# Kernel tuning notes

Measured on AMD Instinct MI355X. Metric: run time of the kernel, lower is better.

The kernel has to match this reference:

```python
import jax, jax.numpy as jnp
import numpy as np

TOP_K = 2  # num_experts_per_tok


def setup_inputs() -> dict:
    key = jax.random.key(0)
    ks = jax.random.split(key, 7)
    B, S, D = 4, 4096, 512
    E, H = 16, 4 * 512  # num_experts, expert hidden dim
    s_in = 1.0 / np.sqrt(D)
    s_h = 1.0 / np.sqrt(H)
    return {
        "x": jax.random.normal(ks[0], (B, S, D), dtype=jnp.float32),
        "Wg": jax.random.normal(ks[1], (D, E), dtype=jnp.float32) * s_in,
        "bg": jnp.zeros((E,), dtype=jnp.float32),
        "W1": jax.random.normal(ks[2], (E, D, H), dtype=jnp.float32) * s_in,
        "b1": jnp.zeros((E, H), dtype=jnp.float32),
        "W2": jax.random.normal(ks[3], (E, H, D), dtype=jnp.float32) * s_h,
        "b2": jnp.zeros((E, D), dtype=jnp.float32),
    }


def reference(x, Wg, bg, W1, b1, W2, b2):
    B, S, D = x.shape
    E = W1.shape[0]
    xf = x.reshape(-1, D)  # [T, D], T = B*S

    # 1. routing: top-k gate logits, softmax over the selected k (in fp32)
    logits = xf @ Wg + bg                      # [T, E]
    w, idx = jax.lax.top_k(logits, TOP_K)      # [T, K]
    w = jax.nn.softmax(w.astype(jnp.float32), axis=1).astype(x.dtype)

    # 2. combine weights per (token, expert): sum of gate weights where selected
    onehot = jax.nn.one_hot(idx, E, dtype=x.dtype)   # [T, K, E]
    combine = jnp.einsum("tk,tke->te", w, onehot)    # [T, E]

    # 3. per-expert FFN (Linear -> GELU(exact) -> Linear), masked combine.
    # Fixed loop over experts (structural, not data dim); tokens not routed to
    # expert e get combine weight 0, matching the sort/segment/scatter original.
    out = jnp.zeros_like(xf)
    for e in range(E):
        h = jax.nn.gelu(xf @ W1[e] + b1[e], approximate=False)  # [T, H]
        y = h @ W2[e] + b2[e]                                   # [T, D]
        out = out + combine[:, e:e + 1] * y

    return out.reshape(B, S, D)
```

## Files before the change

### kernel.cpp

```cpp
#include <hip/hip_runtime.h>
#include <hip/hip_bf16.h>

#define T_TOK 16384
#define DDIM  512
#define NEXP  16
#define HDIM  2048
#define NSLOT (T_TOK * 2)
#define NHB   128

#define GBM 128
#define GBN 256
#define GBN2 128
#define BK  32
#define MAXTILE 272
#define TSLICE  136

typedef __attribute__((ext_vector_type(8))) short short8;
typedef __attribute__((ext_vector_type(4))) short short4v;
typedef __attribute__((ext_vector_type(4))) float f32x4;

__device__ inline short f2bf(float f) {
    __hip_bfloat16 h = __float2bfloat16(f);
    return *reinterpret_cast<short*>(&h);
}
__device__ inline float bf2f(short s) {
    unsigned u = ((unsigned)(unsigned short)s) << 16;
    union { unsigned u; float f; } c; c.u = u; return c.f;
}
__device__ inline float erf_fast(float x) {
    float ax = fabsf(x);
    float t = 1.0f / fmaf(0.3275911f, ax, 1.0f);
    float p = fmaf(fmaf(fmaf(fmaf(1.061405429f, t, -1.453152027f), t,
                  1.421413741f), t, -0.284496736f), t, 0.254829592f) * t;
    float r = 1.0f - p * __expf(-ax * ax);
    return copysignf(r, x);
}
__device__ inline float geluf(float v) {
    return 0.5f * v * (1.0f + erf_fast(v * 0.70710678118654752440f));
}
__device__ inline void gload16(const void* g, void* l) {
    __builtin_amdgcn_global_load_lds(
        (const __attribute__((address_space(1))) void*)g,
        (__attribute__((address_space(3))) void*)l, 16, 0, 0);
}
__device__ inline void xcd_decode(int lin, int nx, int tc, int& y, int& xn) {
    if ((tc & 7) == 0) {
        int tpx = tc >> 3;
        int k = lin & 7, j = lin >> 3;
        y = k * tpx + j % tpx;
        xn = j / tpx;
    } else {
        xn = lin % nx;
        y = lin / nx;
    }
}

__global__ __launch_bounds__(256) void gate_kernel(
    const float* __restrict__ x, const float* __restrict__ wg,
    const float* __restrict__ bg, int* __restrict__ tok_e,
    float* __restrict__ tok_w)
{
    int wv = threadIdx.x >> 6, lane = threadIdx.x & 63;
    int t = blockIdx.x * 4 + wv;
    int g = lane >> 4, q = lane & 15;
    const float* xr = x + (size_t)t * DDIM + g * 128;
    const float* wr = wg + (size_t)g * 128 * NEXP + q;
    double a0 = 0, a1 = 0, a2 = 0, a3 = 0;
#pragma unroll
    for (int c = 0; c < 8; ++c) {
        float4 v0 = ((const float4*)xr)[c * 4 + 0];
        float4 v1 = ((const float4*)xr)[c * 4 + 1];
        float4 v2 = ((const float4*)xr)[c * 4 + 2];
        float4 v3 = ((const float4*)xr)[c * 4 + 3];
        const float* wp = wr + c * 16 * NEXP;
        a0 += (double)v0.x * (double)wp[0 * NEXP];
        a1 += (double)v0.y * (double)wp[1 * NEXP];
        a2 += (double)v0.z * (double)wp[2 * NEXP];
        a3 += (double)v0.w * (double)wp[3 * NEXP];
        a0 += (double)v1.x * (double)wp[4 * NEXP];
        a1 += (double)v1.y * (double)wp[5 * NEXP];
        a2 += (double)v1.z * (double)wp[6 * NEXP];
        a3 += (double)v1.w * (double)wp[7 * NEXP];
        a0 += (double)v2.x * (double)wp[8 * NEXP];
        a1 += (double)v2.y * (double)wp[9 * NEXP];
        a2 += (double)v2.z * (double)wp[10 * NEXP];
        a3 += (double)v2.w * (double)wp[11 * NEXP];
        a0 += (double)v3.x * (double)wp[12 * NEXP];
        a1 += (double)v3.y * (double)wp[13 * NEXP];
        a2 += (double)v3.z * (double)wp[14 * NEXP];
        a3 += (double)v3.w * (double)wp[15 * NEXP];
    }
    double a = ((a0 + a1) + (a2 + a3));
    a += __shfl_xor(a, 16, 64);
    a += __shfl_xor(a, 32, 64);
    a += (double)bg[q];
    double v0 = a; int i0 = q;
#pragma unroll
    for (int s = 1; s < 16; s <<= 1) {
        double ov = __shfl_xor(v0, s, 64);
        int oi = __shfl_xor(i0, s, 64);
        if (ov > v0 || (ov == v0 && oi < i0)) { v0 = ov; i0 = oi; }
    }
    double m2 = (q == i0) ? -1e300 : a;
    double v1 = m2; int i1 = q;
#pragma unroll
    for (int s = 1; s < 16; s <<= 1) {
        double ov = __shfl_xor(v1, s, 64);
        int oi = __shfl_xor(i1, s, 64);
        if (ov > v1 || (ov == v1 && oi < i1)) { v1 = ov; i1 = oi; }
    }
    if (lane == 0) {
        float ex = expf((float)(v1 - v0));
        float w0 = 1.0f / (1.0f + ex);
        tok_e[2 * t] = i0; tok_e[2 * t + 1] = i1;
        tok_w[2 * t] = w0; tok_w[2 * t + 1] = ex * w0;
    }
}

__global__ __launch_bounds__(256) void hist_kernel(
    const int* __restrict__ tok_e, int* __restrict__ bhist)
{
    __shared__ int h[NEXP];
    if (threadIdx.x < NEXP) h[threadIdx.x] = 0;
    __syncthreads();
    atomicAdd(&h[tok_e[blockIdx.x * 256 + threadIdx.x]], 1);
    __syncthreads();
    if (threadIdx.x < NEXP) bhist[blockIdx.x * NEXP + threadIdx.x] = h[threadIdx.x];
}

__global__ void scan_kernel(const int* __restrict__ bhist, int* __restrict__ offs,
                            int* __restrict__ bbase, int* __restrict__ tile_e,
                            int* __restrict__ tile_m0)
{
    int tid = threadIdx.x;
    __shared__ int tot[NEXP];
    if (tid < NEXP) {
        int s = 0;
        for (int b = 0; b < NHB; ++b) s += bhist[b * NEXP + tid];
        tot[tid] = s;
    }
    __syncthreads();
    if (tid == 0) {
        int run = 0;
        for (int e = 0; e < NEXP; ++e) { offs[e] = run; run += tot[e]; }
        offs[NEXP] = run;
        int nt = 0;
        for (int e = 0; e < NEXP; ++e)
            for (int m = offs[e]; m < offs[e + 1]; m += GBM) {
                tile_e[nt] = e; tile_m0[nt] = m; ++nt;
            }
        offs[17] = nt;
    }
    __syncthreads();
    if (tid < NEXP) {
        int run = offs[tid];
        for (int b = 0; b < NHB; ++b) {
            bbase[b * NEXP + tid] = run;
            run += bhist[b * NEXP + tid];
        }
    }
}

__global__ __launch_bounds__(256) void scatter_kernel(
    const int* __restrict__ tok_e, const float* __restrict__ tok_w,
    const int* __restrict__ bbase, int* __restrict__ list_tok,
    float* __restrict__ list_w, int* __restrict__ pos_tk)
{
    __shared__ int h[NEXP];
    if (threadIdx.x < NEXP) h[threadIdx.x] = 0;
    __syncthreads();
    int s = blockIdx.x * 256 + threadIdx.x;
    int e = tok_e[s];
    int r = atomicAdd(&h[e], 1);
    int pos = bbase[blockIdx.x * NEXP + e] + r;
    list_tok[pos] = s >> 1;
    list_w[pos] = tok_w[s];
    pos_tk[s] = pos;
}


__global__ void cvt_bf16_kernel(const float* __restrict__ src, short* __restrict__ dst, int n4)
{
    int i = blockIdx.x * blockDim.x + threadIdx.x;
    int stride = gridDim.x * blockDim.x;
    for (; i < n4; i += stride) {
        float4 v = ((const float4*)src)[i];
        short4v o;
        o[0] = f2bf(v.x); o[1] = f2bf(v.y); o[2] = f2bf(v.z); o[3] = f2bf(v.w);
        ((short4v*)dst)[i] = o;
    }
}

__global__ void wtrans_kernel(const float* __restrict__ src, short* __restrict__ dst, int R, int C)
{
    __shared__ float t[32][33];
    int c0 = blockIdx.x * 32, r0 = blockIdx.y * 32;
    const float* s = src + (size_t)blockIdx.z * R * C;
    short* d = dst + (size_t)blockIdx.z * R * C;
    int cc = threadIdx.x & 31, rr = threadIdx.x >> 5;
#pragma unroll
    for (int pp = 0; pp < 4; ++pp)
        t[rr + pp * 8][cc] = s[(size_t)(r0 + rr + pp * 8) * C + c0 + cc];
    __syncthreads();
#pragma unroll
    for (int pp = 0; pp < 4; ++pp) {
        int c = rr + pp * 8;
        d[(size_t)(c0 + c) * R + r0 + cc] = f2bf(t[cc][c]);
    }
}


__global__ __launch_bounds__(512) void gemm1_kernel(
    const short* __restrict__ xbf, const short* __restrict__ w1t,
    const float* __restrict__ b1, const int* __restrict__ offs,
    const int* __restrict__ tile_e, const int* __restrict__ tile_m0,
    const int* __restrict__ list_tok, short* __restrict__ hbuf,
    int h0, int hlen, int t0, int tc)
{
    int ty, xn;
    xcd_decode((int)blockIdx.x, hlen / GBN, tc, ty, xn);
    int tb = t0 + ty;
    if (tb >= offs[17]) return;
    int e = tile_e[tb], m0 = tile_m0[tb];
    int rows = offs[e + 1] - m0; if (rows > GBM) rows = GBM;
    int n0 = xn * GBN;
    int tid = threadIdx.x, l = tid & 63, w = tid >> 6;

    __shared__ __align__(16) short As[3][GBM * BK];
    __shared__ __align__(16) short Bs[3][GBN * BK];
    __shared__ int ts[GBM];
    if (tid < GBM) ts[tid] = list_tok[m0 + (tid < rows ? tid : rows - 1)];
    __syncthreads();

    int arow = w * 16 + (l >> 2);
    int aslot = (l & 3) ^ ((arow >> 1) & 3);
    const short* gA = xbf + (size_t)ts[arow] * DDIM + aslot * 8;
    int brow0 = (w * 2 + 0) * 16 + (l >> 2);
    int brow1 = (w * 2 + 1) * 16 + (l >> 2);
    int bs0 = (l & 3) ^ ((brow0 >> 1) & 3);
    int bs1 = (l & 3) ^ ((brow1 >> 1) & 3);
    const short* gB0 = w1t + ((size_t)e * HDIM + (size_t)(h0 + n0 + brow0)) * DDIM + bs0 * 8;
    const short* gB1 = w1t + ((size_t)e * HDIM + (size_t)(h0 + n0 + brow1)) * DDIM + bs1 * 8;

    int l15 = l & 15, kq = l >> 4;
    int aoff[4], boff[4];
#pragma unroll
    for (int mi = 0; mi < 4; ++mi) {
        int R = (w >> 2) * 64 + mi * 16 + l15;
        aoff[mi] = R * BK + ((kq ^ ((R >> 1) & 3)) * 8);
    }
#pragma unroll
    for (int ni = 0; ni < 4; ++ni) {
        int S = (w & 3) * 64 + ni * 16 + l15;
        boff[ni] = S * BK + ((kq ^ ((S >> 1) & 3)) * 8);
    }

    f32x4 vzero = {0.0f, 0.0f, 0.0f, 0.0f};
    f32x4 acc[4][4];
#pragma unroll
    for (int i = 0; i < 4; ++i)
#pragma unroll
        for (int j = 0; j < 4; ++j) acc[i][j] = vzero;

#define STAGE1(T, B) {                                            \
        gload16(gA  + (T) * BK, &As[B][w * 512]);                 \
        gload16(gB0 + (T) * BK, &Bs[B][(w * 2 + 0) * 512]);       \
        gload16(gB1 + (T) * BK, &Bs[B][(w * 2 + 1) * 512]); }

    const int nt = DDIM / BK;
    STAGE1(0, 0);
    STAGE1(1, 1);
    int cb = 0, sb = 2;
#pragma unroll 1
    for (int t = 0; t < nt; ++t) {
        if (t < nt - 1) asm volatile("s_waitcnt vmcnt(3)" ::: "memory");
        else            asm volatile("s_waitcnt vmcnt(0)" ::: "memory");
        __builtin_amdgcn_s_barrier();
        __builtin_amdgcn_sched_barrier(0);
        if (t + 2 < nt) STAGE1(t + 2, sb);
        const short* Ab = &As[cb][0];
        const short* Bb = &Bs[cb][0];
        short8 af[4], bv[4];
#pragma unroll
        for (int mi = 0; mi < 4; ++mi) af[mi] = *(const short8*)(Ab + aoff[mi]);
#pragma unroll
        for (int ni = 0; ni < 4; ++ni) bv[ni] = *(const short8*)(Bb + boff[ni]);
        __builtin_amdgcn_s_setprio(1);
#pragma unroll
        for (int mi = 0; mi < 4; ++mi)
#pragma unroll
            for (int ni = 0; ni < 4; ++ni)
                acc[mi][ni] = __builtin_amdgcn_mfma_f32_16x16x32_bf16(
                    af[mi], bv[ni], acc[mi][ni], 0, 0, 0);
        __builtin_amdgcn_s_setprio(0);
        cb = (cb == 2) ? 0 : cb + 1;
        sb = (sb == 2) ? 0 : sb + 1;
    }
#undef STAGE1

    int crow = (w >> 2) * 64 + (kq << 2);
    int ccol = (w & 3) * 64 + l15;
#pragma unroll
    for (int mi = 0; mi < 4; ++mi) {
#pragma unroll
        for (int ni = 0; ni < 4; ++ni) {
            int col = ccol + ni * 16;
            float bias = b1[e * HDIM + h0 + n0 + col];
#pragma unroll
            for (int j = 0; j < 4; ++j) {
                int row = crow + mi * 16 + j;
                if (row < rows) {
                    float v = acc[mi][ni][j] + bias;
                    hbuf[(size_t)(m0 + row) * hlen + (n0 + col)] = f2bf(geluf(v));
                }
            }
        }
    }
}

__global__ __launch_bounds__(512) void gemm2_kernel(
    const short* __restrict__ hbuf, const short* __restrict__ w2t,
    const float* __restrict__ b2, const int* __restrict__ offs,
    const int* __restrict__ tile_e, const int* __restrict__ tile_m0,
    const int* __restrict__ list_tok, const float* __restrict__ list_w,
    short* __restrict__ ybuf, float* __restrict__ out,
    int h0, int hlen, int mode, int t0, int tc)
{
    int ty, xn;
    xcd_decode((int)blockIdx.x, DDIM / GBN2, tc, ty, xn);
    int tb = t0 + ty;
    if (tb >= offs[17]) return;
    int e = tile_e[tb], m0 = tile_m0[tb];
    int rows = offs[e + 1] - m0; if (rows > GBM) rows = GBM;
    int n0 = xn * GBN2;
    int tid = threadIdx.x, l = tid & 63, w = tid >> 6;

    __shared__ __align__(16) short As[3][GBM * BK];
    __shared__ __align__(16) short Bs[3][GBN2 * BK];
    __shared__ int ts[GBM];
    __shared__ float lw[GBM];
    if (tid < GBM) {
        int idx = m0 + (tid < rows ? tid : rows - 1);
        ts[tid] = list_tok[idx];
        lw[tid] = list_w[idx];
    }
    __syncthreads();

    int arow = w * 16 + (l >> 2);
    int aslot = (l & 3) ^ ((arow >> 1) & 3);
    int aslotg = m0 + arow; if (aslotg >= NSLOT) aslotg = NSLOT - 1;
    const short* gA = hbuf + (size_t)aslotg * hlen + aslot * 8;
    int brow = w * 16 + (l >> 2);
    int bslot = (l & 3) ^ ((brow >> 1) & 3);
    const short* gB = w2t + ((size_t)e * DDIM + (size_t)(n0 + brow)) * HDIM + h0 + bslot * 8;

    int l15 = l & 15, kq = l >> 4;
    int aoff[4], boff[2];
#pragma unroll
    for (int mi = 0; mi < 4; ++mi) {
        int R = (w >> 2) * 64 + mi * 16 + l15;
        aoff[mi] = R * BK + ((kq ^ ((R >> 1) & 3)) * 8);
    }
#pragma unroll
    for (int ni = 0; ni < 2; ++ni) {
        int S = (w & 3) * 32 + ni * 16 + l15;
        boff[ni] = S * BK + ((kq ^ ((S >> 1) & 3)) * 8);
    }

    f32x4 vzero = {0.0f, 0.0f, 0.0f, 0.0f};
    f32x4 acc[4][2];
#pragma unroll
    for (int i = 0; i < 4; ++i)
#pragma unroll
        for (int j = 0; j < 2; ++j) acc[i][j] = vzero;

#define STAGE2(T, B) {                                            \
        gload16(gA + (T) * BK, &As[B][w * 512]);                  \
        gload16(gB + (T) * BK, &Bs[B][w * 512]); }

    const int nt = hlen / BK;
    STAGE2(0, 0);
    STAGE2(1, 1);
    int cb = 0, sb = 2;
#pragma unroll 1
    for (int t = 0; t < nt; ++t) {
        if (t < nt - 1) asm volatile("s_waitcnt vmcnt(2)" ::: "memory");
        else            asm volatile("s_waitcnt vmcnt(0)" ::: "memory");
        __builtin_amdgcn_s_barrier();
        __builtin_amdgcn_sched_barrier(0);
        if (t + 2 < nt) STAGE2(t + 2, sb);
        const short* Ab = &As[cb][0];
        const short* Bb = &Bs[cb][0];
        short8 af[4], bv[2];
#pragma unroll
        for (int mi = 0; mi < 4; ++mi) af[mi] = *(const short8*)(Ab + aoff[mi]);
#pragma unroll
        for (int ni = 0; ni < 2; ++ni) bv[ni] = *(const short8*)(Bb + boff[ni]);
        __builtin_amdgcn_s_setprio(1);
#pragma unroll
        for (int mi = 0; mi < 4; ++mi)
#pragma unroll
            for (int ni = 0; ni < 2; ++ni)
                acc[mi][ni] = __builtin_amdgcn_mfma_f32_16x16x32_bf16(
                    af[mi], bv[ni], acc[mi][ni], 0, 0, 0);
        __builtin_amdgcn_s_setprio(0);
        cb = (cb == 2) ? 0 : cb + 1;
        sb = (sb == 2) ? 0 : sb + 1;
    }
#undef STAGE2

    int crow = (w >> 2) * 64 + (kq << 2);
    int ccol = (w & 3) * 32 + l15;
#pragma unroll
    for (int mi = 0; mi < 4; ++mi) {
#pragma unroll
        for (int ni = 0; ni < 2; ++ni) {
            int col = ccol + ni * 16;
            float bias = (h0 == 0) ? b2[e * DDIM + n0 + col] : 0.0f;
#pragma unroll
            for (int j = 0; j < 4; ++j) {
                int row = crow + mi * 16 + j;
                if (row < rows) {
                    float v = acc[mi][ni][j] + bias;
                    if (mode == 0)
                        ybuf[(size_t)(m0 + row) * DDIM + n0 + col] = f2bf(v);
                    else
                        atomicAdd(&out[(size_t)ts[row] * DDIM + n0 + col], lw[row] * v);
                }
            }
        }
    }
}

__global__ __launch_bounds__(256) void combine_kernel(
    const short* __restrict__ ybuf, const int* __restrict__ pos_tk,
    const float* __restrict__ tok_w, float* __restrict__ out)
{
    int i = blockIdx.x * 256 + threadIdx.x;
    int t = i >> 6, c = (i & 63) * 8;
    float w0 = tok_w[2 * t], w1 = tok_w[2 * t + 1];
    int p0 = pos_tk[2 * t], p1 = pos_tk[2 * t + 1];
    short8 a = *(const short8*)(ybuf + (size_t)p0 * DDIM + c);
    short8 b = *(const short8*)(ybuf + (size_t)p1 * DDIM + c);
    float4 o0, o1;
    float* op = (float*)&o0;
#pragma unroll
    for (int j = 0; j < 4; ++j) op[j] = w0 * bf2f(a[j]) + w1 * bf2f(b[j]);
    float* op1 = (float*)&o1;
#pragma unroll
    for (int j = 0; j < 4; ++j) op1[j] = w0 * bf2f(a[4 + j]) + w1 * bf2f(b[4 + j]);
    float4* ob = (float4*)(out + (size_t)t * DDIM + c);
    ob[0] = o0;
    ob[1] = o1;
}


extern "C" void kernel_launch(void* const* d_in, const int* in_sizes, int n_in,
                              void* d_out, int out_size, void* d_ws, size_t ws_size,
                              hipStream_t stream)
{
    const float* x  = (const float*)d_in[0];
    const float* wg = (const float*)d_in[1];
    const float* bg = (const float*)d_in[2];
    const float* w1 = (const float*)d_in[3];
    const float* b1 = (const float*)d_in[4];
    const float* w2 = (const float*)d_in[5];
    const float* b2 = (const float*)d_in[6];
    float* out = (float*)d_out;

    char* p = (char*)d_ws;
    int* offs     = (int*)(p + 128);
    int* tile_e   = (int*)(p + 256);
    int* tile_m0  = (int*)(p + 2304);
    int* bhist    = (int*)(p + 8192);
    int* bbase    = (int*)(p + 16384);
    int* tok_e    = (int*)(p + 32768);
    float* tok_w  = (float*)(p + 32768 + 131072);
    int* list_tok = (int*)(p + 32768 + 262144);
    float* list_w = (float*)(p + 32768 + 393216);
    int* pos_tk   = (int*)(p + 32768 + 524288);
    short* xbf    = (short*)(p + 32768 + 655360);
    short* w1t    = xbf + (size_t)T_TOK * DDIM;
    short* w2t    = w1t + (size_t)NEXP * DDIM * HDIM;
    char* after   = (char*)(w2t + (size_t)NEXP * DDIM * HDIM);
    size_t fixed  = (size_t)(after - p);

    int mode, hlen = HDIM;
    if (fixed + (size_t)NSLOT * DDIM * 2 + (size_t)NSLOT * HDIM * 2 <= ws_size) {
        mode = 0;
    } else {
        mode = 1;
        hlen = 0;
        for (int hl = HDIM; hl >= 128; hl >>= 1)
            if (fixed + (size_t)NSLOT * hl * 2 <= ws_size) { hlen = hl; break; }
    }
    short* ybuf = (short*)after;
    short* hbuf = (mode == 0) ? (short*)(after + (size_t)NSLOT * DDIM * 2) : (short*)after;

    if (!hlen) { hipMemsetAsync(d_out, 0, (size_t)out_size * sizeof(float), stream); return; }
    if (mode == 1) hipMemsetAsync(d_out, 0, (size_t)out_size * sizeof(float), stream);

    gate_kernel<<<T_TOK / 4, 256, 0, stream>>>(x, wg, bg, tok_e, tok_w);
    hist_kernel<<<NHB, 256, 0, stream>>>(tok_e, bhist);
    scan_kernel<<<1, 64, 0, stream>>>(bhist, offs, bbase, tile_e, tile_m0);
    scatter_kernel<<<NHB, 256, 0, stream>>>(tok_e, tok_w, bbase, list_tok, list_w, pos_tk);
    cvt_bf16_kernel<<<2048, 256, 0, stream>>>(x, xbf, T_TOK * DDIM / 4);
    wtrans_kernel<<<dim3(HDIM / 32, DDIM / 32, NEXP), 256, 0, stream>>>(w1, w1t, DDIM, HDIM);
    wtrans_kernel<<<dim3(DDIM / 32, HDIM / 32, NEXP), 256, 0, stream>>>(w2, w2t, HDIM, DDIM);

    for (int h0 = 0; h0 < HDIM; h0 += hlen) {
        for (int t0 = 0; t0 < MAXTILE; t0 += TSLICE) {
            int tc = MAXTILE - t0; if (tc > TSLICE) tc = TSLICE;
            gemm1_kernel<<<(hlen / GBN) * tc, 512, 0, stream>>>(
                xbf, w1t, b1, offs, tile_e, tile_m0, list_tok, hbuf, h0, hlen, t0, tc);
            gemm2_kernel<<<(DDIM / GBN2) * tc, 512, 0, stream>>>(
                hbuf, w2t, b2, offs, tile_e, tile_m0, list_tok, list_w,
                ybuf, out, h0, hlen, mode, t0, tc);
        }
    }
    if (mode == 0)
        combine_kernel<<<T_TOK * 64 / 256, 256, 0, stream>>>(ybuf, pos_tk, tok_w, out);
}
```

Baseline: 400.3 us.

## Switch GEMM kernels from triple-buffered to double-buffered LDS pipeline

Both grouped GEMM kernels now use two LDS stages instead of three. The next tile is prefetched at the start of each iteration, and the loop waits for all loads and a barrier at the end. This lowers LDS usage, which could let more blocks reside per CU. In exchange, prefetch depth drops to one stage, so there is less latency hiding for global loads.

```diff
diff --git a/kernel.cpp b/kernel.cpp
--- a/kernel.cpp
+++ b/kernel.cpp
@@ -226,8 +226,8 @@
     int n0 = xn * GBN;
     int tid = threadIdx.x, l = tid & 63, w = tid >> 6;
 
-    __shared__ __align__(16) short As[3][GBM * BK];
-    __shared__ __align__(16) short Bs[3][GBN * BK];
+    __shared__ __align__(16) short As[2][GBM * BK];
+    __shared__ __align__(16) short Bs[2][GBN * BK];
     __shared__ int ts[GBM];
     if (tid < GBM) ts[tid] = list_tok[m0 + (tid < rows ? tid : rows - 1)];
     __syncthreads();
@@ -269,17 +269,15 @@
 
     const int nt = DDIM / BK;
     STAGE1(0, 0);
-    STAGE1(1, 1);
-    int cb = 0, sb = 2;
+    asm volatile("s_waitcnt vmcnt(0)" ::: "memory");
+    __builtin_amdgcn_s_barrier();
 #pragma unroll 1
     for (int t = 0; t < nt; ++t) {
-        if (t < nt - 1) asm volatile("s_waitcnt vmcnt(3)" ::: "memory");
-        else            asm volatile("s_waitcnt vmcnt(0)" ::: "memory");
-        __builtin_amdgcn_s_barrier();
+        int cur = t & 1;
+        if (t + 1 < nt) STAGE1(t + 1, cur ^ 1);
         __builtin_amdgcn_sched_barrier(0);
-        if (t + 2 < nt) STAGE1(t + 2, sb);
-        const short* Ab = &As[cb][0];
-        const short* Bb = &Bs[cb][0];
+        const short* Ab = &As[cur][0];
+        const short* Bb = &Bs[cur][0];
         short8 af[4], bv[4];
 #pragma unroll
         for (int mi = 0; mi < 4; ++mi) af[mi] = *(const short8*)(Ab + aoff[mi]);
@@ -293,8 +291,10 @@
                 acc[mi][ni] = __builtin_amdgcn_mfma_f32_16x16x32_bf16(
                     af[mi], bv[ni], acc[mi][ni], 0, 0, 0);
         __builtin_amdgcn_s_setprio(0);
-        cb = (cb == 2) ? 0 : cb + 1;
-        sb = (sb == 2) ? 0 : sb + 1;
+        if (t + 1 < nt) {
+            asm volatile("s_waitcnt vmcnt(0)" ::: "memory");
+            __builtin_amdgcn_s_barrier();
+        }
     }
 #undef STAGE1
 
@@ -335,8 +335,8 @@
     int n0 = xn * GBN2;
     int tid = threadIdx.x, l = tid & 63, w = tid >> 6;
 
-    __shared__ __align__(16) short As[3][GBM * BK];
-    __shared__ __align__(16) short Bs[3][GBN2 * BK];
+    __shared__ __align__(16) short As[2][GBM * BK];
+    __shared__ __align__(16) short Bs[2][GBN2 * BK];
     __shared__ int ts[GBM];
     __shared__ float lw[GBM];
     if (tid < GBM) {
@@ -380,17 +380,15 @@
 
     const int nt = hlen / BK;
     STAGE2(0, 0);
-    STAGE2(1, 1);
-    int cb = 0, sb = 2;
+    asm volatile("s_waitcnt vmcnt(0)" ::: "memory");
+    __builtin_amdgcn_s_barrier();
 #pragma unroll 1
     for (int t = 0; t < nt; ++t) {
-        if (t < nt - 1) asm volatile("s_waitcnt vmcnt(2)" ::: "memory");
-        else            asm volatile("s_waitcnt vmcnt(0)" ::: "memory");
-        __builtin_amdgcn_s_barrier();
+        int cur = t & 1;
+        if (t + 1 < nt) STAGE2(t + 1, cur ^ 1);
         __builtin_amdgcn_sched_barrier(0);
-        if (t + 2 < nt) STAGE2(t + 2, sb);
-        const short* Ab = &As[cb][0];
-        const short* Bb = &Bs[cb][0];
+        const short* Ab = &As[cur][0];
+        const short* Bb = &Bs[cur][0];
         short8 af[4], bv[2];
 #pragma unroll
         for (int mi = 0; mi < 4; ++mi) af[mi] = *(const short8*)(Ab + aoff[mi]);
@@ -404,8 +402,10 @@
                 acc[mi][ni] = __builtin_amdgcn_mfma_f32_16x16x32_bf16(
                     af[mi], bv[ni], acc[mi][ni], 0, 0, 0);
         __builtin_amdgcn_s_setprio(0);
-        cb = (cb == 2) ? 0 : cb + 1;
-        sb = (sb == 2) ? 0 : sb + 1;
+        if (t + 1 < nt) {
+            asm volatile("s_waitcnt vmcnt(0)" ::: "memory");
+            __builtin_amdgcn_s_barrier();
+        }
     }
 #undef STAGE2
 
```

Measured after the change: 397.9 us. No clear change (-0.6%).
